# Optimization experiments

Hardware: AMD Instinct MI355X
Metric: run time of the kernel (lower is better)

## Reference

```python
import jax, jax.numpy as jnp
import numpy as np

B, N, D = 16384, 20, 13  # batch of states, agents per state, per-agent joint-state dim
SELF_STATE = 6           # self_state_size in SARL


def setup_inputs() -> dict:
    key = jax.random.key(0)
    ks = jax.random.split(key, 16)

    def init(k, fi, fo):
        # haiku MLP default: truncated-normal-ish std 1/sqrt(fan_in), zero bias
        return jax.random.normal(k, (fi, fo), jnp.float32) / np.float32(np.sqrt(fi))

    z = lambda n: jnp.zeros((n,), jnp.float32)
    return {
        "x": jax.random.normal(ks[0], (B, N, D), jnp.float32),
        # mlp1: 13 -> 150 -> 100, relu, activate_final=True
        "w1a": init(ks[1], D, 150), "b1a": z(150),
        "w1b": init(ks[2], 150, 100), "b1b": z(100),
        # attention: 200 -> 100 -> 100 -> 1
        "wa0": init(ks[3], 200, 100), "ba0": z(100),
        "wa1": init(ks[4], 100, 100), "ba1": z(100),
        "wa2": init(ks[5], 100, 1), "ba2": z(1),
        # mlp2: 100 -> 100 -> 50
        "w2a": init(ks[6], 100, 100), "b2a": z(100),
        "w2b": init(ks[7], 100, 50), "b2b": z(50),
        # mlp3: 56 -> 150 -> 100 -> 100 -> 1
        "w3a": init(ks[8], SELF_STATE + 50, 150), "b3a": z(150),
        "w3b": init(ks[9], 150, 100), "b3b": z(100),
        "w3c": init(ks[10], 100, 100), "b3c": z(100),
        "w3d": init(ks[11], 100, 1), "b3d": z(1),
    }


def reference(x, w1a, b1a, w1b, b1b, wa0, ba0, wa1, ba1, wa2, ba2,
              w2a, b2a, w2b, b2b, w3a, b3a, w3b, b3b, w3c, b3c, w3d, b3d):
    relu = jax.nn.relu
    # mlp1 (activate_final=True): [B,N,100]
    h1 = relu(relu(x @ w1a + b1a) @ w1b + b1b)
    # mean-pool over agents -> global state, broadcast + concat: [B,N,200]
    g = jnp.mean(h1, axis=1, keepdims=True)
    att_in = jnp.concatenate([h1, jnp.broadcast_to(g, h1.shape)], axis=-1)
    # attention MLP -> scores [B,N], softmax over agents
    s = relu(att_in @ wa0 + ba0)
    s = relu(s @ wa1 + ba1)
    scores = (s @ wa2 + ba2)[..., 0]
    attn = jax.nn.softmax(scores, axis=-1)
    # mlp2 features [B,N,50], softmax-weighted sum over agents -> [B,50]
    f = relu(h1 @ w2a + b2a) @ w2b + b2b
    wf = jnp.einsum('bnf,bn->bf', f, attn)
    # concat self-state (first row's first 6 dims) with pooled features -> [B,56]
    self_state = x[:, 0, :SELF_STATE]
    m = jnp.concatenate([self_state, wf], axis=-1)
    # mlp3: 56 -> 150 -> 100 -> 100 -> 1
    h = relu(m @ w3a + b3a)
    h = relu(h @ w3b + b3b)
    h = relu(h @ w3c + b3c)
    return h @ w3d + b3d  # [B,1] state value
```

## Files before the change

kernel.cpp:

```cpp
#include <hip/hip_runtime.h>
#include <math.h>

#define NT     512
#define NWAVES 8
#define GB     4
#define NTOK   20
#define NTT_P  5

typedef _Float16 f16x8 __attribute__((ext_vector_type(8)));
typedef _Float16 f16x4 __attribute__((ext_vector_type(4)));
typedef _Float16 f16x2 __attribute__((ext_vector_type(2)));
typedef float    f32x4 __attribute__((ext_vector_type(4)));

#define PHASE_BAR() do {                                      \
    asm volatile("s_waitcnt lgkmcnt(0)" ::: "memory");        \
    __builtin_amdgcn_s_barrier();                             \
    asm volatile("" ::: "memory");                            \
    __builtin_amdgcn_sched_barrier(0);                        \
} while (0)

#define WS_W1A  0
#define WS_W1B  5120
#define WS_WA0  23040
#define WS_WA1  37376
#define WS_W2A  51712
#define WS_W2B  66048
#define WS_W3A  74240
#define WS_W3B  84480
#define WS_W3C  102400
#define WS_WA0H 116736
#define WS_TOTAL 131072
#define WB_BASE 65536
#define WB_B1A  0
#define WB_B1B  160
#define WB_BA0  272
#define WB_BA1  384
#define WB_B2A  496
#define WB_B2B  608
#define WB_B3A  672
#define WB_B3B  832
#define WB_B3C  944
#define WB_WA2  1056
#define WB_N    1168
#define PREP_TOTAL (WS_TOTAL + WB_N)
#define WS_MV   135168

#define LH_A    0
#define LH_B    12160
#define LH_C    23040
#define LH_T1   LH_A
#define LH_S1   LH_A
#define LH_F1   LH_A
#define LH_H1   LH_B
#define LH_FF   LH_B
#define LH_GQ   LH_C
#define LF_PART 11520
#define LF_GB   12672
#define LF_ATT  13120
#define LF_SS   13200
#define LDS_DW  13224
#define LDS_BYTES (LDS_DW * 4)

#define TB      64
#define TL_MV   0
#define TL_HA   4608
#define TL_HB   15360
#define TL_HC   24064
#define LDS_T_DW   16384
#define LDS_T_BYTES (LDS_T_DW * 4)

__device__ __forceinline__ void prep_one(const float* __restrict__ src, _Float16* dst,
                                         int local, int N, int K, int Ks)
{
    int n = local / Ks, k = local - n * Ks;
    dst[local] = (_Float16)((n < N && k < K) ? src[k * N + n] : 0.f);
}
__device__ __forceinline__ void prep_b(const float* __restrict__ src, float* dst,
                                       int idx, int N)
{
    dst[idx] = (idx < N) ? src[idx] : 0.f;
}

__global__ __launch_bounds__(256)
void prep_kernel(const float* __restrict__ w1a, const float* __restrict__ w1b,
                 const float* __restrict__ wa0, const float* __restrict__ wa1,
                 const float* __restrict__ w2a, const float* __restrict__ w2b,
                 const float* __restrict__ w3a, const float* __restrict__ w3b,
                 const float* __restrict__ w3c, const float* __restrict__ wa2,
                 const float* __restrict__ b1a, const float* __restrict__ b1b,
                 const float* __restrict__ ba0, const float* __restrict__ ba1,
                 const float* __restrict__ b2a, const float* __restrict__ b2b,
                 const float* __restrict__ b3a, const float* __restrict__ b3b,
                 const float* __restrict__ b3c,
                 _Float16* __restrict__ ws)
{
    int g = blockIdx.x * 256 + threadIdx.x;
    if (g >= PREP_TOTAL) return;
    if (g >= WS_TOTAL) {
        float* wb = (float*)ws + WB_BASE;
        int l = g - WS_TOTAL;
        if (l < WB_B1B)      prep_b(b1a, wb + WB_B1A, l - WB_B1A, 150);
        else if (l < WB_BA0) prep_b(b1b, wb + WB_B1B, l - WB_B1B, 100);
        else if (l < WB_BA1) prep_b(ba0, wb + WB_BA0, l - WB_BA0, 100);
        else if (l < WB_B2A) prep_b(ba1, wb + WB_BA1, l - WB_BA1, 100);
        else if (l < WB_B2B) prep_b(b2a, wb + WB_B2A, l - WB_B2A, 100);
        else if (l < WB_B3A) prep_b(b2b, wb + WB_B2B, l - WB_B2B, 50);
        else if (l < WB_B3B) prep_b(b3a, wb + WB_B3A, l - WB_B3A, 150);
        else if (l < WB_B3C) prep_b(b3b, wb + WB_B3B, l - WB_B3B, 100);
        else if (l < WB_WA2) prep_b(b3c, wb + WB_B3C, l - WB_B3C, 100);
        else                 prep_b(wa2, wb + WB_WA2, l - WB_WA2, 100);
        return;
    }
    if (g < WS_W1B)       prep_one(w1a, ws + WS_W1A, g - WS_W1A, 150, 13, 32);
    else if (g < WS_WA0)  prep_one(w1b, ws + WS_W1B, g - WS_W1B, 100, 150, 160);
    else if (g < WS_WA1)  prep_one(wa0, ws + WS_WA0, g - WS_WA0, 100, 100, 128);
    else if (g < WS_W2A)  prep_one(wa1, ws + WS_WA1, g - WS_WA1, 100, 100, 128);
    else if (g < WS_W2B)  prep_one(w2a, ws + WS_W2A, g - WS_W2A, 100, 100, 128);
    else if (g < WS_W3A)  prep_one(w2b, ws + WS_W2B, g - WS_W2B,  50, 100, 128);
    else if (g < WS_W3B)  prep_one(w3a, ws + WS_W3A, g - WS_W3A, 150,  56, 64);
    else if (g < WS_W3C)  prep_one(w3b, ws + WS_W3B, g - WS_W3B, 100, 150, 160);
    else if (g < WS_WA0H) prep_one(w3c, ws + WS_W3C, g - WS_W3C, 100, 100, 128);
    else                  prep_one(wa0 + 100 * 100, ws + WS_WA0H, g - WS_WA0H, 100, 100, 128);
}

template<int KT, int MTL, int NW>
struct WC {
    static constexpr int IPW = (MTL + NW - 1) / NW;
    f16x8 wf[IPW][KT];
    f32x4 bv[IPW];
};

template<int KT, int MTL, int NW, bool LOADB>
__device__ __forceinline__ void load_w(WC<KT, MTL, NW>& W,
                                       const _Float16* __restrict__ WT, const int Bs,
                                       const float* __restrict__ biasp,
                                       const int wv, const int lane)
{
    const int cl = lane & 15, kq = lane >> 4;
#pragma unroll
    for (int ii = 0; ii < WC<KT, MTL, NW>::IPW; ++ii) {
        const int mt = wv + ii * NW;
        if (mt < MTL) {
            const _Float16* Wp = WT + (mt * 16 + cl) * Bs + kq * 8;
#pragma unroll
            for (int kt = 0; kt < KT; ++kt) W.wf[ii][kt] = *(const f16x8*)(Wp + kt * 32);
            if (LOADB) W.bv[ii] = *(const f32x4*)(biasp + mt * 16 + kq * 4);
        }
    }
}

template<int KT, int MTL, int NTT, bool RELU, int BMODE, int OMODE, int CLW, int NW>
__device__ __forceinline__ void gemm_c(const WC<KT, MTL, NW>& W,
                                       const _Float16* X, const int Xs,
                                       const float* gbias,
                                       _Float16* Y, const int Ys,
                                       float* part, const float* __restrict__ wa2p,
                                       const int wv, const int lane)
{
    const int cl = lane & 15, kq = lane >> 4;
#pragma unroll
    for (int ii = 0; ii < WC<KT, MTL, NW>::IPW; ++ii) {
        const int mt = wv + ii * NW;
        if (mt >= MTL) break;
        const int fb = mt * 16 + kq * 4;
#pragma unroll
        for (int nt = 0; nt < NTT; ++nt) {
            const _Float16* Xp = X + (nt * 16 + cl) * Xs + kq * 8;
            f16x8 xf[KT];
#pragma unroll
            for (int kt = 0; kt < KT; ++kt) xf[kt] = *(const f16x8*)(Xp + kt * 32);
            f32x4 acc = {0.f, 0.f, 0.f, 0.f};
#pragma unroll
            for (int kt = 0; kt < KT; ++kt)
                acc = __builtin_amdgcn_mfma_f32_16x16x32_f16(W.wf[ii][kt], xf[kt], acc, 0, 0, 0);
            const int token = nt * 16 + cl;
            if (OMODE == 1) {
                if (cl < GB) {
                    f32x4 o = acc + W.bv[ii];
                    *(f32x4*)((float*)Y + cl * 112 + fb) = o;
                }
            } else if (OMODE == 2) {
                f32x4 y = acc + W.bv[ii];
                y[0] = fmaxf(y[0], 0.f); y[1] = fmaxf(y[1], 0.f);
                y[2] = fmaxf(y[2], 0.f); y[3] = fmaxf(y[3], 0.f);
                f32x4 w4 = *(const f32x4*)(wa2p + fb);
                float p = y[0] * w4[0] + y[1] * w4[1] + y[2] * w4[2] + y[3] * w4[3];
                p += __shfl_xor(p, 16);
                p += __shfl_xor(p, 32);
                if (kq == 0) part[token * 8 + mt] = p;
            } else {
                f32x4 bb;
                if (BMODE == 1)
                    bb = *(const f32x4*)(gbias + (token / NTOK) * 112 + fb);
                else
                    bb = W.bv[ii];
                f32x4 y = acc + bb;
                if (RELU) {
                    y[0] = fmaxf(y[0], 0.f); y[1] = fmaxf(y[1], 0.f);
                    y[2] = fmaxf(y[2], 0.f); y[3] = fmaxf(y[3], 0.f);
                }
                if (fb < CLW) {
                    f16x4 o = { (_Float16)y[0], (_Float16)y[1],
                                (_Float16)y[2], (_Float16)y[3] };
                    *(f16x4*)(Y + token * Ys + fb) = o;
                }
            }
        }
    }
}

__global__ __launch_bounds__(NT, 6)
void vnet_kernel(const float* __restrict__ x,
                 const float* __restrict__ ba2,
                 const _Float16* __restrict__ wsh,
                 _Float16* __restrict__ mvg)
{
    extern __shared__ float lds_f[];
    _Float16* lds_h = (_Float16*)lds_f;

    const int tid  = threadIdx.x;
    const int lane = tid & 63, wv = tid >> 6;
    const int b0   = blockIdx.x * GB;
    const float* wb = (const float*)wsh + WB_BASE;

    _Float16* xa  = lds_h + LH_C;
    _Float16* gqh = lds_h + LH_GQ;
    _Float16* h1w = lds_h + LH_H1;
    float* gbias = lds_f + LF_GB;
    float* att   = lds_f + LF_ATT;
    float* ss    = lds_f + LF_SS;
    float* part  = lds_f + LF_PART;

    WC<1, 10, 8> Wp2;
    WC<5, 7, 8>  Wp3;
    WC<4, 7, 8>  Wmg;
    WC<4, 7, 8>  Wm1;
    WC<4, 7, 8>  Wm2;
    WC<4, 7, 8>  Wm3;
    WC<4, 4, 4>  Wm4;

    load_w<1, 10, 8, true>(Wp2, wsh + WS_W1A, 32, wb + WB_B1A, wv, lane);
    const float* xg = x + (size_t)b0 * (NTOK * 13);
    for (int t = tid; t < GB * NTOK * 13; t += NT) {
        int row = t / 13, d = t - row * 13;
        xa[row * 40 + d] = (_Float16)xg[t];
    }
    for (int t = tid; t < 80 * 27; t += NT) {
        int row = t / 27, c = 13 + (t - row * 27);
        xa[row * 40 + c] = (_Float16)0.f;
    }
    for (int t = tid; t < 80 * 24; t += NT) {
        int row = t / 24, c = 112 + (t - row * 24);
        h1w[row * 136 + c] = (_Float16)0.f;
    }
    if (tid < 8) h1w[tid] = (_Float16)0.f;
    if (tid < GB * 6) {
        int b = tid / 6, d = tid - b * 6;
        ss[tid] = xg[b * (NTOK * 13) + d];
    }
    PHASE_BAR();

    load_w<5, 7, 8, true>(Wp3, wsh + WS_W1B, 160, wb + WB_B1B, wv, lane);
    gemm_c<1, 10, NTT_P, true, 0, 0, 152, 8>(Wp2, xa, 40, nullptr,
        lds_h + LH_T1, 152, nullptr, nullptr, wv, lane);
    PHASE_BAR();

    load_w<4, 7, 8, true>(Wmg, wsh + WS_WA0H, 128, wb + WB_BA0, wv, lane);
    gemm_c<5, 7, NTT_P, true, 0, 0, 10000, 8>(Wp3, lds_h + LH_T1, 152, nullptr,
        h1w, 136, nullptr, nullptr, wv, lane);
    PHASE_BAR();

    load_w<4, 7, 8, false>(Wm1, wsh + WS_WA0, 128, nullptr, wv, lane);
    const _Float16* h1 = h1w;
    const uint* h1u = (const uint*)h1;
    for (int t = tid; t < GB * 50; t += NT) {
        int b = t / 50, cp = t - b * 50;
        float s0 = 0.f, s1 = 0.f;
#pragma unroll
        for (int n = 0; n < NTOK; ++n) {
            uint v = h1u[(b * NTOK + n) * 68 + cp];
            f16x2 p = *(const f16x2*)&v;
            s0 += (float)p.x; s1 += (float)p.y;
        }
        f16x2 g = { (_Float16)(s0 * 0.05f), (_Float16)(s1 * 0.05f) };
        *(f16x2*)(gqh + b * 136 + 2 * cp) = g;
    }
    PHASE_BAR();

    load_w<4, 7, 8, true>(Wm2, wsh + WS_WA1, 128, wb + WB_BA1, wv, lane);
    gemm_c<4, 7, 1, false, 0, 1, 10000, 8>(Wmg, gqh, 136, nullptr,
        (_Float16*)gbias, 0, nullptr, nullptr, wv, lane);
    PHASE_BAR();

    load_w<4, 7, 8, true>(Wm3, wsh + WS_W2A, 128, wb + WB_B2A, wv, lane);
    gemm_c<4, 7, NTT_P, true, 1, 0, 10000, 8>(Wm1, h1, 136, gbias,
        lds_h + LH_S1, 136, nullptr, nullptr, wv, lane);
    PHASE_BAR();

    load_w<4, 4, 4, true>(Wm4, wsh + WS_W2B, 128, wb + WB_B2B, wv, lane);
    gemm_c<4, 7, NTT_P, true, 0, 2, 10000, 8>(Wm2, lds_h + LH_S1, 136, nullptr,
        nullptr, 0, part, wb + WB_WA2, wv, lane);
    PHASE_BAR();

    gemm_c<4, 7, NTT_P, true, 0, 0, 10000, 8>(Wm3, h1, 136, nullptr,
        lds_h + LH_F1, 136, nullptr, nullptr, wv, lane);
    PHASE_BAR();

    if (wv < 4) {
        gemm_c<4, 4, NTT_P, false, 0, 0, 10000, 4>(Wm4, lds_h + LH_F1, 136,
            nullptr, lds_h + LH_FF, 72, nullptr, nullptr, wv, lane);
    } else {
        const int b = wv - 4;
        float sc = -1e30f;
        if (lane < NTOK) {
            sc = ba2[0];
            const float* pr = part + (b * NTOK + lane) * 8;
#pragma unroll
            for (int m = 0; m < 7; ++m) sc += pr[m];
        }
        float mx = sc;
#pragma unroll
        for (int off = 16; off; off >>= 1) mx = fmaxf(mx, __shfl_xor(mx, off, 32));
        float e = (lane < NTOK) ? expf(sc - mx) : 0.f;
        float s = e;
#pragma unroll
        for (int off = 16; off; off >>= 1) s += __shfl_xor(s, off, 32);
        if (lane < NTOK) att[b * NTOK + lane] = e / s;
    }
    PHASE_BAR();

    const _Float16* fh = lds_h + LH_FF;
    for (int t = tid; t < GB * 64; t += NT) {
        int b = t >> 6, c = t & 63;
        float v = 0.f;
        if (c < 6) {
            v = ss[b * 6 + c];
        } else if (c < 56) {
            const int cc = c - 6;
            const float* ab = att + b * NTOK;
            float acc = 0.f;
#pragma unroll
            for (int n = 0; n < NTOK; ++n)
                acc = fmaf((float)fh[(b * NTOK + n) * 72 + cc], ab[n], acc);
            v = acc;
        }
        mvg[(size_t)(b0 + b) * 64 + c] = (_Float16)v;
    }
}

__global__ __launch_bounds__(NT)
void tail_kernel(const _Float16* __restrict__ mvg,
                 const float* __restrict__ w3d, const float* __restrict__ b3d,
                 const _Float16* __restrict__ wsh,
                 float* __restrict__ outp)
{
    extern __shared__ float lds_f[];
    _Float16* lds_h = (_Float16*)lds_f;

    const int tid  = threadIdx.x;
    const int lane = tid & 63, wv = tid >> 6;
    const int g0   = blockIdx.x * TB;
    const float* wb = (const float*)wsh + WB_BASE;

    WC<2, 10, 8> Wt1; WC<5, 7, 8> Wt2; WC<4, 7, 8> Wt3;
    load_w<2, 10, 8, true>(Wt1, wsh + WS_W3A, 64, wb + WB_B3A, wv, lane);

    _Float16* mvT = lds_h + TL_MV;
    {
        const uint* src = (const uint*)(mvg + (size_t)g0 * 64);
        uint* dst = (uint*)mvT;
        for (int t = tid; t < TB * 32; t += NT) {
            int row = t >> 5, c = t & 31;
            dst[row * 36 + c] = src[t];
        }
    }
    for (int t = tid; t < (TL_HC - TL_HB) / 2; t += NT)
        ((uint*)(lds_h + TL_HB))[t] = 0u;
    __syncthreads();

    load_w<5, 7, 8, true>(Wt2, wsh + WS_W3B, 160, wb + WB_B3B, wv, lane);
    gemm_c<2, 10, 4, true, 0, 0, 10000, 8>(Wt1, mvT, 72, nullptr,
        lds_h + TL_HA, 168, nullptr, nullptr, wv, lane);
    __syncthreads();

    load_w<4, 7, 8, true>(Wt3, wsh + WS_W3C, 128, wb + WB_B3C, wv, lane);
    gemm_c<5, 7, 4, true, 0, 0, 10000, 8>(Wt2, lds_h + TL_HA, 168, nullptr,
        lds_h + TL_HB, 136, nullptr, nullptr, wv, lane);
    __syncthreads();

    gemm_c<4, 7, 4, true, 0, 0, 10000, 8>(Wt3, lds_h + TL_HB, 136, nullptr,
        lds_h + TL_HC, 136, nullptr, nullptr, wv, lane);
    __syncthreads();

    {
        const int b = tid >> 3, kl = tid & 7;
        const _Float16* hc = lds_h + TL_HC + b * 136;
        float acc = 0.f;
#pragma unroll 13
        for (int k = kl; k < 100; k += 8)
            acc = fmaf((float)hc[k], w3d[k], acc);
        acc += __shfl_xor(acc, 1);
        acc += __shfl_xor(acc, 2);
        acc += __shfl_xor(acc, 4);
        if (kl == 0) outp[g0 + b] = acc + b3d[0];
    }
}

extern "C" void kernel_launch(void* const* d_in, const int* in_sizes, int n_in,
                              void* d_out, int out_size, void* d_ws, size_t ws_size,
                              hipStream_t stream)
{
    const float* x   = (const float*)d_in[0];
    const float* w1a = (const float*)d_in[1];
    const float* b1a = (const float*)d_in[2];
    const float* w1b = (const float*)d_in[3];
    const float* b1b = (const float*)d_in[4];
    const float* wa0 = (const float*)d_in[5];
    const float* ba0 = (const float*)d_in[6];
    const float* wa1 = (const float*)d_in[7];
    const float* ba1 = (const float*)d_in[8];
    const float* wa2 = (const float*)d_in[9];
    const float* ba2 = (const float*)d_in[10];
    const float* w2a = (const float*)d_in[11];
    const float* b2a = (const float*)d_in[12];
    const float* w2b = (const float*)d_in[13];
    const float* b2b = (const float*)d_in[14];
    const float* w3a = (const float*)d_in[15];
    const float* b3a = (const float*)d_in[16];
    const float* w3b = (const float*)d_in[17];
    const float* b3b = (const float*)d_in[18];
    const float* w3c = (const float*)d_in[19];
    const float* b3c = (const float*)d_in[20];
    const float* w3d = (const float*)d_in[21];
    const float* b3d = (const float*)d_in[22];
    float* outp = (float*)d_out;
    _Float16* wsh = (_Float16*)d_ws;
    _Float16* mvg = wsh + WS_MV;

    hipFuncSetAttribute((const void*)vnet_kernel,
                        hipFuncAttributeMaxDynamicSharedMemorySize, LDS_BYTES);
    hipFuncSetAttribute((const void*)tail_kernel,
                        hipFuncAttributeMaxDynamicSharedMemorySize, LDS_T_BYTES);

    hipLaunchKernelGGL(prep_kernel, dim3((PREP_TOTAL + 255) / 256), dim3(256),
                       0, stream,
                       w1a, w1b, wa0, wa1, w2a, w2b, w3a, w3b, w3c, wa2,
                       b1a, b1b, ba0, ba1, b2a, b2b, b3a, b3b, b3c, wsh);

    const int B = 16384;
    hipLaunchKernelGGL(vnet_kernel, dim3(B / GB), dim3(NT), LDS_BYTES, stream,
                       x, ba2, wsh, mvg);
    hipLaunchKernelGGL(tail_kernel, dim3(B / TB), dim3(NT), LDS_T_BYTES, stream,
                       mvg, w3d, b3d, wsh, outp);
}
```

Measured before the change: 133.9 us.

## Load late-stage weights just in time and drop a barrier between global-bias GEMMs

Removes the prefetched weight-register holders for the attention-1, mlp2a and mlp2b layers and instead loads each layer's weights right before its GEMM through a new gemm_sw helper. This lowers register pressure and may allow higher occupancy, at the cost of exposing global weight-load latency. The block barrier between the global-bias GEMM and the first attention GEMM is replaced by a wave-local LDS wait. The tail kernel switches to a simplified GEMM helper without bias-mode or column-limit branches.

```diff
diff --git a/kernel.cpp b/kernel.cpp
--- a/kernel.cpp
+++ b/kernel.cpp
@@ -15,6 +15,12 @@
 #define PHASE_BAR() do {                                      \
     asm volatile("s_waitcnt lgkmcnt(0)" ::: "memory");        \
     __builtin_amdgcn_s_barrier();                             \
+    asm volatile("" ::: "memory");                            \
+    __builtin_amdgcn_sched_barrier(0);                        \
+} while (0)
+
+#define WAVE_BAR() do {                                       \
+    asm volatile("s_waitcnt lgkmcnt(0)" ::: "memory");        \
     asm volatile("" ::: "memory");                            \
     __builtin_amdgcn_sched_barrier(0);                        \
 } while (0)
@@ -209,6 +215,21 @@
     }
 }
 
+template<int KT, int MTL, int NTT, bool RELU, int BMODE, int OMODE, int CLW, int NW>
+__device__ __forceinline__ void gemm_sw(const _Float16* X, const int Xs,
+                                        const _Float16* __restrict__ WT, const int Bs,
+                                        const float* __restrict__ biasp,
+                                        const float* gbias,
+                                        _Float16* Y, const int Ys,
+                                        float* part, const float* __restrict__ wa2p,
+                                        const int wv, const int lane)
+{
+    WC<KT, MTL, NW> W;
+    load_w<KT, MTL, NW, true>(W, WT, Bs, biasp ? biasp : (const float*)WT, wv, lane);
+    gemm_c<KT, MTL, NTT, RELU, BMODE, OMODE, CLW, NW>(W, X, Xs, gbias, Y, Ys,
+                                                      part, wa2p, wv, lane);
+}
+
 __global__ __launch_bounds__(NT, 6)
 void vnet_kernel(const float* __restrict__ x,
                  const float* __restrict__ ba2,
@@ -233,11 +254,8 @@
 
     WC<1, 10, 8> Wp2;
     WC<5, 7, 8>  Wp3;
-    WC<4, 7, 8>  Wmg;
+    WC<4, 7, 8>  Wg;
     WC<4, 7, 8>  Wm1;
-    WC<4, 7, 8>  Wm2;
-    WC<4, 7, 8>  Wm3;
-    WC<4, 4, 4>  Wm4;
 
     load_w<1, 10, 8, true>(Wp2, wsh + WS_W1A, 32, wb + WB_B1A, wv, lane);
     const float* xg = x + (size_t)b0 * (NTOK * 13);
@@ -265,11 +283,11 @@
         lds_h + LH_T1, 152, nullptr, nullptr, wv, lane);
     PHASE_BAR();
 
-    load_w<4, 7, 8, true>(Wmg, wsh + WS_WA0H, 128, wb + WB_BA0, wv, lane);
     gemm_c<5, 7, NTT_P, true, 0, 0, 10000, 8>(Wp3, lds_h + LH_T1, 152, nullptr,
         h1w, 136, nullptr, nullptr, wv, lane);
     PHASE_BAR();
 
+    load_w<4, 7, 8, true>(Wg, wsh + WS_WA0H, 128, wb + WB_BA0, wv, lane);
     load_w<4, 7, 8, false>(Wm1, wsh + WS_WA0, 128, nullptr, wv, lane);
     const _Float16* h1 = h1w;
     const uint* h1u = (const uint*)h1;
@@ -279,36 +297,33 @@
 #pragma unroll
         for (int n = 0; n < NTOK; ++n) {
             uint v = h1u[(b * NTOK + n) * 68 + cp];
-            f16x2 p = *(const f16x2*)&v;
-            s0 += (float)p.x; s1 += (float)p.y;
+            f16x2 pq = *(const f16x2*)&v;
+            s0 += (float)pq.x; s1 += (float)pq.y;
         }
         f16x2 g = { (_Float16)(s0 * 0.05f), (_Float16)(s1 * 0.05f) };
         *(f16x2*)(gqh + b * 136 + 2 * cp) = g;
     }
     PHASE_BAR();
 
-    load_w<4, 7, 8, true>(Wm2, wsh + WS_WA1, 128, wb + WB_BA1, wv, lane);
-    gemm_c<4, 7, 1, false, 0, 1, 10000, 8>(Wmg, gqh, 136, nullptr,
+    gemm_c<4, 7, 1, false, 0, 1, 10000, 8>(Wg, gqh, 136, nullptr,
         (_Float16*)gbias, 0, nullptr, nullptr, wv, lane);
-    PHASE_BAR();
-
-    load_w<4, 7, 8, true>(Wm3, wsh + WS_W2A, 128, wb + WB_B2A, wv, lane);
+    WAVE_BAR();
     gemm_c<4, 7, NTT_P, true, 1, 0, 10000, 8>(Wm1, h1, 136, gbias,
         lds_h + LH_S1, 136, nullptr, nullptr, wv, lane);
     PHASE_BAR();
 
-    load_w<4, 4, 4, true>(Wm4, wsh + WS_W2B, 128, wb + WB_B2B, wv, lane);
-    gemm_c<4, 7, NTT_P, true, 0, 2, 10000, 8>(Wm2, lds_h + LH_S1, 136, nullptr,
-        nullptr, 0, part, wb + WB_WA2, wv, lane);
-    PHASE_BAR();
-
-    gemm_c<4, 7, NTT_P, true, 0, 0, 10000, 8>(Wm3, h1, 136, nullptr,
-        lds_h + LH_F1, 136, nullptr, nullptr, wv, lane);
+    gemm_sw<4, 7, NTT_P, true, 0, 2, 10000, 8>(lds_h + LH_S1, 136, wsh + WS_WA1,
+        128, wb + WB_BA1, nullptr, nullptr, 0, part, wb + WB_WA2, wv, lane);
+    PHASE_BAR();
+
+    gemm_sw<4, 7, NTT_P, true, 0, 0, 10000, 8>(h1, 136, wsh + WS_W2A, 128,
+        wb + WB_B2A, nullptr, lds_h + LH_F1, 136, nullptr, nullptr, wv, lane);
     PHASE_BAR();
 
     if (wv < 4) {
-        gemm_c<4, 4, NTT_P, false, 0, 0, 10000, 4>(Wm4, lds_h + LH_F1, 136,
-            nullptr, lds_h + LH_FF, 72, nullptr, nullptr, wv, lane);
+        gemm_sw<4, 4, NTT_P, false, 0, 0, 10000, 4>(lds_h + LH_F1, 136,
+            wsh + WS_W2B, 128, wb + WB_B2B, nullptr, lds_h + LH_FF, 72,
+            nullptr, nullptr, wv, lane);
     } else {
         const int b = wv - 4;
         float sc = -1e30f;
@@ -348,6 +363,41 @@
     }
 }
 
+template<int KT, int MTL, int NTT, bool RELU, int NW>
+__device__ __forceinline__ void gemm_wc(const WC<KT, MTL, NW>& W,
+                                        const _Float16* X, const int Xs,
+                                        _Float16* Y, const int Ys,
+                                        const int wv, const int lane)
+{
+    const int cl = lane & 15, kq = lane >> 4;
+#pragma unroll
+    for (int ii = 0; ii < WC<KT, MTL, NW>::IPW; ++ii) {
+        const int mt = wv + ii * NW;
+        if (mt >= MTL) break;
+        const int fb = mt * 16 + kq * 4;
+#pragma unroll
+        for (int nt = 0; nt < NTT; ++nt) {
+            const _Float16* Xp = X + (nt * 16 + cl) * Xs + kq * 8;
+            f16x8 xf[KT];
+#pragma unroll
+            for (int kt = 0; kt < KT; ++kt) xf[kt] = *(const f16x8*)(Xp + kt * 32);
+            f32x4 acc = {0.f, 0.f, 0.f, 0.f};
+#pragma unroll
+            for (int kt = 0; kt < KT; ++kt)
+                acc = __builtin_amdgcn_mfma_f32_16x16x32_f16(W.wf[ii][kt], xf[kt], acc, 0, 0, 0);
+            const int token = nt * 16 + cl;
+            f32x4 y = acc + W.bv[ii];
+            if (RELU) {
+                y[0] = fmaxf(y[0], 0.f); y[1] = fmaxf(y[1], 0.f);
+                y[2] = fmaxf(y[2], 0.f); y[3] = fmaxf(y[3], 0.f);
+            }
+            f16x4 o = { (_Float16)y[0], (_Float16)y[1],
+                        (_Float16)y[2], (_Float16)y[3] };
+            *(f16x4*)(Y + token * Ys + fb) = o;
+        }
+    }
+}
+
 __global__ __launch_bounds__(NT)
 void tail_kernel(const _Float16* __restrict__ mvg,
                  const float* __restrict__ w3d, const float* __restrict__ b3d,
@@ -379,17 +429,14 @@
     __syncthreads();
 
     load_w<5, 7, 8, true>(Wt2, wsh + WS_W3B, 160, wb + WB_B3B, wv, lane);
-    gemm_c<2, 10, 4, true, 0, 0, 10000, 8>(Wt1, mvT, 72, nullptr,
-        lds_h + TL_HA, 168, nullptr, nullptr, wv, lane);
+    gemm_wc<2, 10, 4, true, 8>(Wt1, mvT, 72, lds_h + TL_HA, 168, wv, lane);
     __syncthreads();
 
     load_w<4, 7, 8, true>(Wt3, wsh + WS_W3C, 128, wb + WB_B3C, wv, lane);
-    gemm_c<5, 7, 4, true, 0, 0, 10000, 8>(Wt2, lds_h + TL_HA, 168, nullptr,
-        lds_h + TL_HB, 136, nullptr, nullptr, wv, lane);
+    gemm_wc<5, 7, 4, true, 8>(Wt2, lds_h + TL_HA, 168, lds_h + TL_HB, 136, wv, lane);
     __syncthreads();
 
-    gemm_c<4, 7, 4, true, 0, 0, 10000, 8>(Wt3, lds_h + TL_HB, 136, nullptr,
-        lds_h + TL_HC, 136, nullptr, nullptr, wv, lane);
+    gemm_wc<4, 7, 4, true, 8>(Wt3, lds_h + TL_HB, 136, lds_h + TL_HC, 136, wv, lane);
     __syncthreads();
 
     {
```

Result: faster. 115.8 us (-13.6%).
